# Performance work log

Hardware: AMD Instinct MI355X
Metric: run time of the kernel (lower is better)

Reference implementation:

```python
import jax, jax.numpy as jnp
import numpy as np

B, H, S = 128, 512, 2048

def setup_inputs() -> dict:
    key = jax.random.key(0)
    ks = jax.random.split(key, 8)
    sc = 1.0 / np.sqrt(H)
    return {
        "all_hidden": jax.random.normal(ks[0], (B, H, S), dtype=jnp.float32),
        "v_att": jax.random.normal(ks[1], (H,), dtype=jnp.float32) * sc,
        "W_att": jax.random.normal(ks[2], (H, H), dtype=jnp.float32) * sc,
        "v_ptr": jax.random.normal(ks[3], (H,), dtype=jnp.float32) * sc,
        "fc1_w": jax.random.normal(ks[4], (H, H), dtype=jnp.float32) * sc,
        "fc1_b": jax.random.normal(ks[5], (H,), dtype=jnp.float32) * sc,
        "fc2_w": jax.random.normal(ks[6], (H, H), dtype=jnp.float32) * sc,
        "fc2_b": jax.random.normal(ks[7], (H,), dtype=jnp.float32) * sc,
    }

def reference(all_hidden, v_att, W_att, v_ptr, fc1_w, fc1_b, fc2_w, fc2_b):
    # all_hidden: [B, H, S]
    # Attention: attns = softmax(v . tanh(W @ all_hidden), over seq)
    scores = jnp.einsum('hk,bks->bhs', W_att, all_hidden)          # [B,H,S]
    attn = jax.nn.softmax(jnp.einsum('h,bhs->bs', v_att, jnp.tanh(scores)), axis=-1)  # [B,S]
    # context = attn @ all_hidden^T  -> [B,H]
    context = jnp.einsum('bs,bhs->bh', attn, all_hidden)
    # 2-layer MLP with relu (torch Linear: x @ W^T + b)
    out = jax.nn.relu(context @ fc1_w.T + fc1_b)
    out = jax.nn.relu(out @ fc2_w.T + fc2_b)                        # [B,H]
    # probs = v . tanh(all_hidden + out broadcast over seq)
    probs = jnp.einsum('h,bhs->bs', v_ptr, jnp.tanh(all_hidden + out[:, :, None]))  # [B,S]
    return probs
```

## Files before the change

kernel.cpp:

```cpp
#include <hip/hip_runtime.h>
#include <hip/hip_bf16.h>

#define B_ 128
#define H_ 512
#define S_ 2048
#define ST 64
#define NP (S_/ST)
#define RB 520

typedef short  bf16x8  __attribute__((ext_vector_type(8)));
typedef float  floatx4 __attribute__((ext_vector_type(4)));

__device__ __forceinline__ unsigned short f2bf(float f){
  unsigned u = __float_as_uint(f);
  unsigned r = (u + 0x7fffu + ((u >> 16) & 1u)) >> 16;
  return (unsigned short)r;
}
__device__ __forceinline__ float bf2f(unsigned short h){
  return __uint_as_float(((unsigned)h) << 16);
}
__device__ __forceinline__ float fast_tanh(float x){
  x = fminf(15.f, fmaxf(-15.f, x));
  float e = __expf(2.f * x);
  return (e - 1.f) * __builtin_amdgcn_rcpf(e + 1.f);
}

typedef short short4v __attribute__((ext_vector_type(4)));
__global__ __launch_bounds__(256) void k_convW(const float* __restrict__ W,
                                               unsigned short* __restrict__ Wb){
  int i = (blockIdx.x * 256 + threadIdx.x) * 4;
  float4 v = *(const float4*)(W + i);
  short4v o;
  o[0] = (short)f2bf(v.x); o[1] = (short)f2bf(v.y);
  o[2] = (short)f2bf(v.z); o[3] = (short)f2bf(v.w);
  *(short4v*)(Wb + i) = o;
}

__global__ __launch_bounds__(256, 2) void k_pass1(
    const float* __restrict__ hidden, const float* __restrict__ v_att,
    const unsigned short* __restrict__ Wb,
    float* __restrict__ part_m, float* __restrict__ part_z,
    float* __restrict__ part_ctx)
{
  __shared__ unsigned short Bs[ST * RB];
  __shared__ float vatt[H_];
  __shared__ float twav[4][ST];
  __shared__ float ts[ST];
  __shared__ float es[ST];

  const int tid = threadIdx.x;
  const int w = tid >> 6, l = tid & 63;
  const int p = blockIdx.x & (NP - 1);
  const int b = blockIdx.x >> 5;
  const int s0 = p * ST;

  vatt[tid]       = v_att[tid];
  vatt[tid + 256] = v_att[tid + 256];

  {
    const float* src0 = hidden + ((size_t)b * H_) * S_ + s0 + l;
    #pragma unroll
    for (int it = 0; it < 16; ++it){
      int kb = it * 32 + w * 8;
      const float* src = src0 + (size_t)kb * S_;
      bf16x8 pk;
      #pragma unroll
      for (int j = 0; j < 8; ++j)
        pk[j] = (short)f2bf(src[(size_t)j * S_]);
      *(bf16x8*)(&Bs[l * RB + kb]) = pk;
    }
  }
  __syncthreads();

  const int quad = l >> 4, l16 = l & 15;
  float tacc[4] = {0.f, 0.f, 0.f, 0.f};

  for (int o = 0; o < 2; ++o){
    const int htbase = w * 8 + o * 4;
    floatx4 acc[4][4];
    #pragma unroll
    for (int ti = 0; ti < 4; ++ti)
      #pragma unroll
      for (int ss = 0; ss < 4; ++ss){
        floatx4 z4 = {0.f, 0.f, 0.f, 0.f};
        acc[ti][ss] = z4;
      }

    for (int k0 = 0; k0 < H_; k0 += 32){
      bf16x8 a[4];
      #pragma unroll
      for (int ti = 0; ti < 4; ++ti)
        a[ti] = *(const bf16x8*)(Wb + ((htbase + ti) * 16 + l16) * H_ + k0 + quad * 8);
      bf16x8 bb[4];
      #pragma unroll
      for (int ss = 0; ss < 4; ++ss)
        bb[ss] = *(const bf16x8*)(&Bs[(ss * 16 + l16) * RB + k0 + quad * 8]);
      #pragma unroll
      for (int ti = 0; ti < 4; ++ti)
        #pragma unroll
        for (int ss = 0; ss < 4; ++ss)
          acc[ti][ss] = __builtin_amdgcn_mfma_f32_16x16x32_bf16(a[ti], bb[ss], acc[ti][ss], 0, 0, 0);
    }

    #pragma unroll
    for (int ti = 0; ti < 4; ++ti){
      const int hbase = (htbase + ti) * 16 + quad * 4;
      #pragma unroll
      for (int r = 0; r < 4; ++r){
        float va = vatt[hbase + r];
        #pragma unroll
        for (int ss = 0; ss < 4; ++ss)
          tacc[ss] += va * fast_tanh(acc[ti][ss][r]);
      }
    }
  }

  #pragma unroll
  for (int ss = 0; ss < 4; ++ss){
    tacc[ss] += __shfl_xor(tacc[ss], 16);
    tacc[ss] += __shfl_xor(tacc[ss], 32);
  }
  if (l < 16){
    #pragma unroll
    for (int ss = 0; ss < 4; ++ss) twav[w][ss * 16 + l] = tacc[ss];
  }
  __syncthreads();
  if (tid < ST) ts[tid] = twav[0][tid] + twav[1][tid] + twav[2][tid] + twav[3][tid];
  __syncthreads();

  float m = -1e30f;
  for (int s = 0; s < ST; ++s) m = fmaxf(m, ts[s]);
  if (tid < ST) es[tid] = __expf(ts[tid] - m);
  __syncthreads();
  float z = 0.f;
  for (int s = 0; s < ST; ++s) z += es[s];

  const int pidx = b * NP + p;
  if (tid == 0){ part_m[pidx] = m; part_z[pidx] = z; }

  for (int h = tid; h < H_; h += 256){
    float a = 0.f;
    for (int s = 0; s < ST; ++s) a += es[s] * bf2f(Bs[s * RB + h]);
    part_ctx[(size_t)pidx * H_ + h] = a;
  }
}

__global__ __launch_bounds__(256) void k_mlp(
    const float* __restrict__ part_m, const float* __restrict__ part_z,
    const float* __restrict__ part_ctx,
    const float* __restrict__ fc1_w, const float* __restrict__ fc1_b,
    const float* __restrict__ fc2_w, const float* __restrict__ fc2_b,
    float* __restrict__ out2)
{
  __shared__ float ctx[H_];
  __shared__ float h1[H_];
  __shared__ float wp[NP];
  const int b = blockIdx.x, tid = threadIdx.x;

  float m = -1e30f;
  for (int pp = 0; pp < NP; ++pp) m = fmaxf(m, part_m[b * NP + pp]);
  if (tid < NP) wp[tid] = __expf(part_m[b * NP + tid] - m);
  __syncthreads();
  float z = 0.f;
  for (int pp = 0; pp < NP; ++pp) z += wp[pp] * part_z[b * NP + pp];
  float invz = 1.f / z;

  for (int h = tid; h < H_; h += 256){
    float a = 0.f;
    for (int pp = 0; pp < NP; ++pp) a += wp[pp] * part_ctx[(size_t)(b * NP + pp) * H_ + h];
    ctx[h] = a * invz;
  }
  __syncthreads();

  for (int i = tid; i < H_; i += 256){
    const float4* row = (const float4*)(fc1_w + (size_t)i * H_);
    float4 s4 = {0.f, 0.f, 0.f, 0.f};
    for (int j = 0; j < H_ / 4; ++j){
      float4 wv = row[j];
      s4.x += wv.x * ctx[4 * j];     s4.y += wv.y * ctx[4 * j + 1];
      s4.z += wv.z * ctx[4 * j + 2]; s4.w += wv.w * ctx[4 * j + 3];
    }
    h1[i] = fmaxf(fc1_b[i] + s4.x + s4.y + s4.z + s4.w, 0.f);
  }
  __syncthreads();

  for (int i = tid; i < H_; i += 256){
    const float4* row = (const float4*)(fc2_w + (size_t)i * H_);
    float4 s4 = {0.f, 0.f, 0.f, 0.f};
    for (int j = 0; j < H_ / 4; ++j){
      float4 wv = row[j];
      s4.x += wv.x * h1[4 * j];     s4.y += wv.y * h1[4 * j + 1];
      s4.z += wv.z * h1[4 * j + 2]; s4.w += wv.w * h1[4 * j + 3];
    }
    out2[(size_t)b * H_ + i] = fmaxf(fc2_b[i] + s4.x + s4.y + s4.z + s4.w, 0.f);
  }
}

__global__ __launch_bounds__(256) void k_probs(
    const float* __restrict__ hidden, const float* __restrict__ v_ptr,
    const float* __restrict__ out2, float* __restrict__ probs)
{
  __shared__ float vp[H_], ob[H_];
  const int b = blockIdx.y, c = blockIdx.x, tid = threadIdx.x;
  vp[tid]       = v_ptr[tid];
  vp[tid + 256] = v_ptr[tid + 256];
  ob[tid]       = out2[(size_t)b * H_ + tid];
  ob[tid + 256] = out2[(size_t)b * H_ + tid + 256];
  __syncthreads();

  const int s = c * 512 + tid * 2;
  const float* base = hidden + (size_t)b * H_ * S_ + s;
  float a0 = 0.f, a1 = 0.f;
  #pragma unroll 4
  for (int h = 0; h < H_; ++h){
    float2 hv = *(const float2*)(base + (size_t)h * S_);
    float wv = vp[h], o = ob[h];
    a0 += wv * fast_tanh(hv.x + o);
    a1 += wv * fast_tanh(hv.y + o);
  }
  probs[(size_t)b * S_ + s]     = a0;
  probs[(size_t)b * S_ + s + 1] = a1;
}

extern "C" void kernel_launch(void* const* d_in, const int* in_sizes, int n_in,
                              void* d_out, int out_size, void* d_ws, size_t ws_size,
                              hipStream_t stream)
{
  const float* hidden = (const float*)d_in[0];
  const float* v_att  = (const float*)d_in[1];
  const float* W_att  = (const float*)d_in[2];
  const float* v_ptr  = (const float*)d_in[3];
  const float* fc1_w  = (const float*)d_in[4];
  const float* fc1_b  = (const float*)d_in[5];
  const float* fc2_w  = (const float*)d_in[6];
  const float* fc2_b  = (const float*)d_in[7];
  float* probs = (float*)d_out;

  char* ws = (char*)d_ws;
  unsigned short* Wb = (unsigned short*)ws;
  float* part_m   = (float*)(ws + 524288);
  float* part_z   = (float*)(ws + 524288 + 16384);
  float* part_ctx = (float*)(ws + 524288 + 32768);
  float* out2     = (float*)(ws + 524288 + 32768 + 8388608);

  hipLaunchKernelGGL(k_convW, dim3(256), dim3(256), 0, stream, W_att, Wb);
  hipLaunchKernelGGL(k_pass1, dim3(B_ * NP), dim3(256), 0, stream,
                     hidden, v_att, Wb, part_m, part_z, part_ctx);
  hipLaunchKernelGGL(k_mlp, dim3(B_), dim3(256), 0, stream,
                     part_m, part_z, part_ctx, fc1_w, fc1_b, fc2_w, fc2_b, out2);
  hipLaunchKernelGGL(k_probs, dim3(4, B_), dim3(256), 0, stream,
                     hidden, v_ptr, out2, probs);
}
```

Before: 1.136 ms.

## Pre-transpose hidden to bf16 [B,S,H] and use it in attention and pointer passes

```diff
diff --git a/kernel.cpp b/kernel.cpp
--- a/kernel.cpp
+++ b/kernel.cpp
@@ -10,6 +10,7 @@
 
 typedef short  bf16x8  __attribute__((ext_vector_type(8)));
 typedef float  floatx4 __attribute__((ext_vector_type(4)));
+typedef short  short4v __attribute__((ext_vector_type(4)));
 
 __device__ __forceinline__ unsigned short f2bf(float f){
   unsigned u = __float_as_uint(f);
@@ -25,7 +26,6 @@
   return (e - 1.f) * __builtin_amdgcn_rcpf(e + 1.f);
 }
 
-typedef short short4v __attribute__((ext_vector_type(4)));
 __global__ __launch_bounds__(256) void k_convW(const float* __restrict__ W,
                                                unsigned short* __restrict__ Wb){
   int i = (blockIdx.x * 256 + threadIdx.x) * 4;
@@ -36,26 +36,156 @@
   *(short4v*)(Wb + i) = o;
 }
 
-__global__ __launch_bounds__(256, 2) void k_pass1(
+__global__ __launch_bounds__(256) void k_trans(const float* __restrict__ hidden,
+                                               unsigned short* __restrict__ hT){
+  const int tid = threadIdx.x, w = tid >> 6, l = tid & 63;
+  const int b = blockIdx.y, s0 = blockIdx.x * 64;
+  const float* src = hidden + (size_t)b * H_ * S_ + s0 + l;
+  unsigned short* dst = hT + ((size_t)(b * S_) + s0 + l) * H_;
+  #pragma unroll 4
+  for (int it = 0; it < 16; ++it){
+    int h0 = it * 32 + w * 8;
+    bf16x8 pk;
+    #pragma unroll
+    for (int j = 0; j < 8; ++j)
+      pk[j] = (short)f2bf(src[(size_t)(h0 + j) * S_]);
+    *(bf16x8*)(dst + h0) = pk;
+  }
+}
+
+struct Pass1Shared {
+  unsigned short Bs[ST * RB];
+  float vatt[H_];
+  float twav[4][ST];
+  float ts[ST];
+  float es[ST];
+};
+
+__device__ __forceinline__ void pass1_core(Pass1Shared& sh,
+    const unsigned short* __restrict__ Wb,
+    float* __restrict__ part_m, float* __restrict__ part_z,
+    float* __restrict__ part_ctx, int b, int p)
+{
+  const int tid = threadIdx.x;
+  const int w = tid >> 6, l = tid & 63;
+  const int quad = l >> 4, l16 = l & 15;
+  float tacc[4] = {0.f, 0.f, 0.f, 0.f};
+
+  for (int o = 0; o < 2; ++o){
+    const int htbase = w * 8 + o * 4;
+    floatx4 acc[4][4];
+    #pragma unroll
+    for (int ti = 0; ti < 4; ++ti)
+      #pragma unroll
+      for (int ss = 0; ss < 4; ++ss){
+        floatx4 z4 = {0.f, 0.f, 0.f, 0.f};
+        acc[ti][ss] = z4;
+      }
+
+    for (int k0 = 0; k0 < H_; k0 += 32){
+      bf16x8 a[4];
+      #pragma unroll
+      for (int ti = 0; ti < 4; ++ti)
+        a[ti] = *(const bf16x8*)(Wb + ((htbase + ti) * 16 + l16) * H_ + k0 + quad * 8);
+      bf16x8 bb[4];
+      #pragma unroll
+      for (int ss = 0; ss < 4; ++ss)
+        bb[ss] = *(const bf16x8*)(&sh.Bs[(ss * 16 + l16) * RB + k0 + quad * 8]);
+      #pragma unroll
+      for (int ti = 0; ti < 4; ++ti)
+        #pragma unroll
+        for (int ss = 0; ss < 4; ++ss)
+          acc[ti][ss] = __builtin_amdgcn_mfma_f32_16x16x32_bf16(a[ti], bb[ss], acc[ti][ss], 0, 0, 0);
+    }
+
+    #pragma unroll
+    for (int ti = 0; ti < 4; ++ti){
+      const int hbase = (htbase + ti) * 16 + quad * 4;
+      #pragma unroll
+      for (int r = 0; r < 4; ++r){
+        float va = sh.vatt[hbase + r];
+        #pragma unroll
+        for (int ss = 0; ss < 4; ++ss)
+          tacc[ss] += va * fast_tanh(acc[ti][ss][r]);
+      }
+    }
+  }
+
+  #pragma unroll
+  for (int ss = 0; ss < 4; ++ss){
+    tacc[ss] += __shfl_xor(tacc[ss], 16);
+    tacc[ss] += __shfl_xor(tacc[ss], 32);
+  }
+  if (l < 16){
+    #pragma unroll
+    for (int ss = 0; ss < 4; ++ss) sh.twav[w][ss * 16 + l] = tacc[ss];
+  }
+  __syncthreads();
+  if (tid < ST) sh.ts[tid] = sh.twav[0][tid] + sh.twav[1][tid] + sh.twav[2][tid] + sh.twav[3][tid];
+  __syncthreads();
+
+  float m = -1e30f;
+  for (int s = 0; s < ST; ++s) m = fmaxf(m, sh.ts[s]);
+  if (tid < ST) sh.es[tid] = __expf(sh.ts[tid] - m);
+  __syncthreads();
+  float z = 0.f;
+  for (int s = 0; s < ST; ++s) z += sh.es[s];
+
+  const int pidx = b * NP + p;
+  if (tid == 0){ part_m[pidx] = m; part_z[pidx] = z; }
+
+  for (int h = tid; h < H_; h += 256){
+    float a = 0.f;
+    for (int s = 0; s < ST; ++s) a += sh.es[s] * bf2f(sh.Bs[s * RB + h]);
+    part_ctx[(size_t)pidx * H_ + h] = a;
+  }
+}
+
+__global__ __launch_bounds__(256, 2) void k_pass1_hT(
+    const unsigned short* __restrict__ hT, const float* __restrict__ v_att,
+    const unsigned short* __restrict__ Wb,
+    float* __restrict__ part_m, float* __restrict__ part_z,
+    float* __restrict__ part_ctx)
+{
+  __shared__ Pass1Shared sh;
+  const int tid = threadIdx.x, w = tid >> 6, l = tid & 63;
+  const int p = blockIdx.x & (NP - 1);
+  const int b = blockIdx.x >> 5;
+  const int s0 = p * ST;
+
+  sh.vatt[tid]       = v_att[tid];
+  sh.vatt[tid + 256] = v_att[tid + 256];
+
+  const unsigned short* src = hT + (size_t)(b * S_ + s0) * H_;
+  #pragma unroll
+  for (int r = 0; r < 2; ++r){
+    const int s = w * 16 + (l >> 3) * 2 + r;
+    const unsigned short* row = src + (size_t)s * H_;
+    #pragma unroll
+    for (int i = 0; i < 8; ++i){
+      const int c8 = ((l & 7) + 8 * i) * 8;
+      bf16x8 v = *(const bf16x8*)(row + c8);
+      *(bf16x8*)(&sh.Bs[s * RB + c8]) = v;
+    }
+  }
+  __syncthreads();
+  pass1_core(sh, Wb, part_m, part_z, part_ctx, b, p);
+}
+
+__global__ __launch_bounds__(256, 2) void k_pass1_f32(
     const float* __restrict__ hidden, const float* __restrict__ v_att,
     const unsigned short* __restrict__ Wb,
     float* __restrict__ part_m, float* __restrict__ part_z,
     float* __restrict__ part_ctx)
 {
-  __shared__ unsigned short Bs[ST * RB];
-  __shared__ float vatt[H_];
-  __shared__ float twav[4][ST];
-  __shared__ float ts[ST];
-  __shared__ float es[ST];
-
-  const int tid = threadIdx.x;
-  const int w = tid >> 6, l = tid & 63;
+  __shared__ Pass1Shared sh;
+  const int tid = threadIdx.x, w = tid >> 6, l = tid & 63;
   const int p = blockIdx.x & (NP - 1);
   const int b = blockIdx.x >> 5;
   const int s0 = p * ST;
 
-  vatt[tid]       = v_att[tid];
-  vatt[tid + 256] = v_att[tid + 256];
+  sh.vatt[tid]       = v_att[tid];
+  sh.vatt[tid + 256] = v_att[tid + 256];
 
   {
     const float* src0 = hidden + ((size_t)b * H_) * S_ + s0 + l;
@@ -67,82 +197,11 @@
       #pragma unroll
       for (int j = 0; j < 8; ++j)
         pk[j] = (short)f2bf(src[(size_t)j * S_]);
-      *(bf16x8*)(&Bs[l * RB + kb]) = pk;
-    }
-  }
-  __syncthreads();
-
-  const int quad = l >> 4, l16 = l & 15;
-  float tacc[4] = {0.f, 0.f, 0.f, 0.f};
-
-  for (int o = 0; o < 2; ++o){
-    const int htbase = w * 8 + o * 4;
-    floatx4 acc[4][4];
-    #pragma unroll
-    for (int ti = 0; ti < 4; ++ti)
-      #pragma unroll
-      for (int ss = 0; ss < 4; ++ss){
-        floatx4 z4 = {0.f, 0.f, 0.f, 0.f};
-        acc[ti][ss] = z4;
-      }
-
-    for (int k0 = 0; k0 < H_; k0 += 32){
-      bf16x8 a[4];
-      #pragma unroll
-      for (int ti = 0; ti < 4; ++ti)
-        a[ti] = *(const bf16x8*)(Wb + ((htbase + ti) * 16 + l16) * H_ + k0 + quad * 8);
-      bf16x8 bb[4];
-      #pragma unroll
-      for (int ss = 0; ss < 4; ++ss)
-        bb[ss] = *(const bf16x8*)(&Bs[(ss * 16 + l16) * RB + k0 + quad * 8]);
-      #pragma unroll
-      for (int ti = 0; ti < 4; ++ti)
-        #pragma unroll
-        for (int ss = 0; ss < 4; ++ss)
-          acc[ti][ss] = __builtin_amdgcn_mfma_f32_16x16x32_bf16(a[ti], bb[ss], acc[ti][ss], 0, 0, 0);
-    }
-
-    #pragma unroll
-    for (int ti = 0; ti < 4; ++ti){
-      const int hbase = (htbase + ti) * 16 + quad * 4;
-      #pragma unroll
-      for (int r = 0; r < 4; ++r){
-        float va = vatt[hbase + r];
-        #pragma unroll
-        for (int ss = 0; ss < 4; ++ss)
-          tacc[ss] += va * fast_tanh(acc[ti][ss][r]);
-      }
-    }
-  }
-
-  #pragma unroll
-  for (int ss = 0; ss < 4; ++ss){
-    tacc[ss] += __shfl_xor(tacc[ss], 16);
-    tacc[ss] += __shfl_xor(tacc[ss], 32);
-  }
-  if (l < 16){
-    #pragma unroll
-    for (int ss = 0; ss < 4; ++ss) twav[w][ss * 16 + l] = tacc[ss];
-  }
-  __syncthreads();
-  if (tid < ST) ts[tid] = twav[0][tid] + twav[1][tid] + twav[2][tid] + twav[3][tid];
-  __syncthreads();
-
-  float m = -1e30f;
-  for (int s = 0; s < ST; ++s) m = fmaxf(m, ts[s]);
-  if (tid < ST) es[tid] = __expf(ts[tid] - m);
-  __syncthreads();
-  float z = 0.f;
-  for (int s = 0; s < ST; ++s) z += es[s];
-
-  const int pidx = b * NP + p;
-  if (tid == 0){ part_m[pidx] = m; part_z[pidx] = z; }
-
-  for (int h = tid; h < H_; h += 256){
-    float a = 0.f;
-    for (int s = 0; s < ST; ++s) a += es[s] * bf2f(Bs[s * RB + h]);
-    part_ctx[(size_t)pidx * H_ + h] = a;
-  }
+      *(bf16x8*)(&sh.Bs[l * RB + kb]) = pk;
+    }
+  }
+  __syncthreads();
+  pass1_core(sh, Wb, part_m, part_z, part_ctx, b, p);
 }
 
 __global__ __launch_bounds__(256) void k_mlp(
@@ -196,7 +255,42 @@
   }
 }
 
-__global__ __launch_bounds__(256) void k_probs(
+__global__ __launch_bounds__(256) void k_probs_hT(
+    const unsigned short* __restrict__ hT, const float* __restrict__ v_ptr,
+    const float* __restrict__ out2, float* __restrict__ probs)
+{
+  const int tid = threadIdx.x, w = tid >> 6, l = tid & 63;
+  const int b = blockIdx.y, s0 = blockIdx.x * 64;
+
+  float vp[8], ob[8];
+  {
+    float4 a = *(const float4*)(v_ptr + l * 8);
+    float4 c = *(const float4*)(v_ptr + l * 8 + 4);
+    vp[0]=a.x; vp[1]=a.y; vp[2]=a.z; vp[3]=a.w;
+    vp[4]=c.x; vp[5]=c.y; vp[6]=c.z; vp[7]=c.w;
+    float4 d = *(const float4*)(out2 + (size_t)b * H_ + l * 8);
+    float4 e = *(const float4*)(out2 + (size_t)b * H_ + l * 8 + 4);
+    ob[0]=d.x; ob[1]=d.y; ob[2]=d.z; ob[3]=d.w;
+    ob[4]=e.x; ob[5]=e.y; ob[6]=e.z; ob[7]=e.w;
+  }
+
+  const unsigned short* base = hT + (size_t)(b * S_ + s0) * H_ + l * 8;
+  #pragma unroll 2
+  for (int i = 0; i < 16; ++i){
+    const int s = w * 16 + i;
+    bf16x8 hv = *(const bf16x8*)(base + (size_t)s * H_);
+    float acc = 0.f;
+    #pragma unroll
+    for (int j = 0; j < 8; ++j)
+      acc += vp[j] * fast_tanh(bf2f((unsigned short)hv[j]) + ob[j]);
+    acc += __shfl_xor(acc, 1);  acc += __shfl_xor(acc, 2);
+    acc += __shfl_xor(acc, 4);  acc += __shfl_xor(acc, 8);
+    acc += __shfl_xor(acc, 16); acc += __shfl_xor(acc, 32);
+    if (l == 0) probs[(size_t)b * S_ + s0 + s] = acc;
+  }
+}
+
+__global__ __launch_bounds__(256) void k_probs_f32(
     const float* __restrict__ hidden, const float* __restrict__ v_ptr,
     const float* __restrict__ out2, float* __restrict__ probs)
 {
@@ -238,16 +332,30 @@
 
   char* ws = (char*)d_ws;
   unsigned short* Wb = (unsigned short*)ws;
-  float* part_m   = (float*)(ws + 524288);
-  float* part_z   = (float*)(ws + 524288 + 16384);
-  float* part_ctx = (float*)(ws + 524288 + 32768);
-  float* out2     = (float*)(ws + 524288 + 32768 + 8388608);
+  float* part_m   = (float*)(ws + (512u<<10));
+  float* part_z   = (float*)(ws + (512u<<10) + (16u<<10));
+  float* part_ctx = (float*)(ws + (512u<<10) + (32u<<10));
+  float* out2     = (float*)(ws + (512u<<10) + (32u<<10) + (8u<<20));
+  unsigned short* hT = (unsigned short*)(ws + (16u<<20));
+
+  const size_t need = (16u<<20) + ((size_t)B_ * S_ * H_ * 2);
 
   hipLaunchKernelGGL(k_convW, dim3(256), dim3(256), 0, stream, W_att, Wb);
-  hipLaunchKernelGGL(k_pass1, dim3(B_ * NP), dim3(256), 0, stream,
-                     hidden, v_att, Wb, part_m, part_z, part_ctx);
-  hipLaunchKernelGGL(k_mlp, dim3(B_), dim3(256), 0, stream,
-                     part_m, part_z, part_ctx, fc1_w, fc1_b, fc2_w, fc2_b, out2);
-  hipLaunchKernelGGL(k_probs, dim3(4, B_), dim3(256), 0, stream,
-                     hidden, v_ptr, out2, probs);
-}
+
+  if (ws_size >= need){
+    hipLaunchKernelGGL(k_trans, dim3(S_/64, B_), dim3(256), 0, stream, hidden, hT);
+    hipLaunchKernelGGL(k_pass1_hT, dim3(B_ * NP), dim3(256), 0, stream,
+                       hT, v_att, Wb, part_m, part_z, part_ctx);
+    hipLaunchKernelGGL(k_mlp, dim3(B_), dim3(256), 0, stream,
+                       part_m, part_z, part_ctx, fc1_w, fc1_b, fc2_w, fc2_b, out2);
+    hipLaunchKernelGGL(k_probs_hT, dim3(S_/64, B_), dim3(256), 0, stream,
+                       hT, v_ptr, out2, probs);
+  } else {
+    hipLaunchKernelGGL(k_pass1_f32, dim3(B_ * NP), dim3(256), 0, stream,
+                       hidden, v_att, Wb, part_m, part_z, part_ctx);
+    hipLaunchKernelGGL(k_mlp, dim3(B_), dim3(256), 0, stream,
+                       part_m, part_z, part_ctx, fc1_w, fc1_b, fc2_w, fc2_b, out2);
+    hipLaunchKernelGGL(k_probs_f32, dim3(4, B_), dim3(256), 0, stream,
+                       hidden, v_ptr, out2, probs);
+  }
+}
```

Measured after the change: 1.503 ms. 1.32x slower.

## Write bf16 transposed hidden in pass1 and read it in probs kernel

Applied to the files above, without the earlier changes.

```diff
diff --git a/kernel.cpp b/kernel.cpp
--- a/kernel.cpp
+++ b/kernel.cpp
@@ -6,10 +6,10 @@
 #define S_ 2048
 #define ST 64
 #define NP (S_/ST)
-#define RB 520
 
 typedef short  bf16x8  __attribute__((ext_vector_type(8)));
 typedef float  floatx4 __attribute__((ext_vector_type(4)));
+typedef short  short4v __attribute__((ext_vector_type(4)));
 
 __device__ __forceinline__ unsigned short f2bf(float f){
   unsigned u = __float_as_uint(f);
@@ -24,8 +24,10 @@
   float e = __expf(2.f * x);
   return (e - 1.f) * __builtin_amdgcn_rcpf(e + 1.f);
 }
-
-typedef short short4v __attribute__((ext_vector_type(4)));
+__device__ __forceinline__ int swz(int s, int c){
+  return (c & 56) | ((c ^ s) & 7);
+}
+
 __global__ __launch_bounds__(256) void k_convW(const float* __restrict__ W,
                                                unsigned short* __restrict__ Wb){
   int i = (blockIdx.x * 256 + threadIdx.x) * 4;
@@ -36,15 +38,16 @@
   *(short4v*)(Wb + i) = o;
 }
 
-__global__ __launch_bounds__(256, 2) void k_pass1(
+template<int WRITE_HT>
+__global__ __launch_bounds__(512, 4) void k_pass1(
     const float* __restrict__ hidden, const float* __restrict__ v_att,
     const unsigned short* __restrict__ Wb,
     float* __restrict__ part_m, float* __restrict__ part_z,
-    float* __restrict__ part_ctx)
-{
-  __shared__ unsigned short Bs[ST * RB];
+    float* __restrict__ part_ctx, unsigned short* __restrict__ hT)
+{
+  __shared__ unsigned short Bs[ST * 512];
   __shared__ float vatt[H_];
-  __shared__ float twav[4][ST];
+  __shared__ float twav[8][ST];
   __shared__ float ts[ST];
   __shared__ float es[ST];
 
@@ -54,29 +57,37 @@
   const int b = blockIdx.x >> 5;
   const int s0 = p * ST;
 
-  vatt[tid]       = v_att[tid];
-  vatt[tid + 256] = v_att[tid + 256];
+  vatt[tid] = v_att[tid];
 
   {
     const float* src0 = hidden + ((size_t)b * H_) * S_ + s0 + l;
     #pragma unroll
-    for (int it = 0; it < 16; ++it){
-      int kb = it * 32 + w * 8;
-      const float* src = src0 + (size_t)kb * S_;
+    for (int it = 0; it < 8; ++it){
+      const int c = w + it * 8;
+      const float* src = src0 + (size_t)(c * 8) * S_;
       bf16x8 pk;
       #pragma unroll
       for (int j = 0; j < 8; ++j)
-        pk[j] = (short)f2bf(src[(size_t)j * S_]);
-      *(bf16x8*)(&Bs[l * RB + kb]) = pk;
-    }
-  }
-  __syncthreads();
+        pk[j] = (short)f2bf(__builtin_nontemporal_load(src + (size_t)j * S_));
+      *(bf16x8*)(&Bs[l * 512 + swz(l, c) * 8]) = pk;
+    }
+  }
+  __syncthreads();
+
+  if (WRITE_HT){
+    #pragma unroll
+    for (int r = 0; r < 8; ++r){
+      const int s = w * 8 + r;
+      bf16x8 v = *(const bf16x8*)(&Bs[s * 512 + swz(s, l) * 8]);
+      __builtin_nontemporal_store(v,
+          (bf16x8*)(hT + ((size_t)(b * S_) + s0 + s) * H_ + l * 8));
+    }
+  }
 
   const int quad = l >> 4, l16 = l & 15;
   float tacc[4] = {0.f, 0.f, 0.f, 0.f};
 
-  for (int o = 0; o < 2; ++o){
-    const int htbase = w * 8 + o * 4;
+  {
     floatx4 acc[4][4];
     #pragma unroll
     for (int ti = 0; ti < 4; ++ti)
@@ -90,11 +101,13 @@
       bf16x8 a[4];
       #pragma unroll
       for (int ti = 0; ti < 4; ++ti)
-        a[ti] = *(const bf16x8*)(Wb + ((htbase + ti) * 16 + l16) * H_ + k0 + quad * 8);
+        a[ti] = *(const bf16x8*)(Wb + ((w * 4 + ti) * 16 + l16) * H_ + k0 + quad * 8);
       bf16x8 bb[4];
       #pragma unroll
-      for (int ss = 0; ss < 4; ++ss)
-        bb[ss] = *(const bf16x8*)(&Bs[(ss * 16 + l16) * RB + k0 + quad * 8]);
+      for (int ss = 0; ss < 4; ++ss){
+        const int c = (k0 >> 3) + quad;
+        bb[ss] = *(const bf16x8*)(&Bs[(ss * 16 + l16) * 512 + swz(l16, c) * 8]);
+      }
       #pragma unroll
       for (int ti = 0; ti < 4; ++ti)
         #pragma unroll
@@ -104,7 +117,7 @@
 
     #pragma unroll
     for (int ti = 0; ti < 4; ++ti){
-      const int hbase = (htbase + ti) * 16 + quad * 4;
+      const int hbase = (w * 4 + ti) * 16 + quad * 4;
       #pragma unroll
       for (int r = 0; r < 4; ++r){
         float va = vatt[hbase + r];
@@ -125,7 +138,12 @@
     for (int ss = 0; ss < 4; ++ss) twav[w][ss * 16 + l] = tacc[ss];
   }
   __syncthreads();
-  if (tid < ST) ts[tid] = twav[0][tid] + twav[1][tid] + twav[2][tid] + twav[3][tid];
+  if (tid < ST){
+    float a = 0.f;
+    #pragma unroll
+    for (int ww = 0; ww < 8; ++ww) a += twav[ww][tid];
+    ts[tid] = a;
+  }
   __syncthreads();
 
   float m = -1e30f;
@@ -138,10 +156,12 @@
   const int pidx = b * NP + p;
   if (tid == 0){ part_m[pidx] = m; part_z[pidx] = z; }
 
-  for (int h = tid; h < H_; h += 256){
+  {
+    const int c = tid >> 3, e = tid & 7;
     float a = 0.f;
-    for (int s = 0; s < ST; ++s) a += es[s] * bf2f(Bs[s * RB + h]);
-    part_ctx[(size_t)pidx * H_ + h] = a;
+    for (int s = 0; s < ST; ++s)
+      a += es[s] * bf2f(Bs[s * 512 + swz(s, c) * 8 + e]);
+    part_ctx[(size_t)pidx * H_ + tid] = a;
   }
 }
 
@@ -196,7 +216,42 @@
   }
 }
 
-__global__ __launch_bounds__(256) void k_probs(
+__global__ __launch_bounds__(256) void k_probs_hT(
+    const unsigned short* __restrict__ hT, const float* __restrict__ v_ptr,
+    const float* __restrict__ out2, float* __restrict__ probs)
+{
+  const int tid = threadIdx.x, w = tid >> 6, l = tid & 63;
+  const int b = blockIdx.y, s0 = blockIdx.x * 64;
+
+  float vp[8], ob[8];
+  {
+    float4 a = *(const float4*)(v_ptr + l * 8);
+    float4 c = *(const float4*)(v_ptr + l * 8 + 4);
+    vp[0]=a.x; vp[1]=a.y; vp[2]=a.z; vp[3]=a.w;
+    vp[4]=c.x; vp[5]=c.y; vp[6]=c.z; vp[7]=c.w;
+    float4 d = *(const float4*)(out2 + (size_t)b * H_ + l * 8);
+    float4 e = *(const float4*)(out2 + (size_t)b * H_ + l * 8 + 4);
+    ob[0]=d.x; ob[1]=d.y; ob[2]=d.z; ob[3]=d.w;
+    ob[4]=e.x; ob[5]=e.y; ob[6]=e.z; ob[7]=e.w;
+  }
+
+  const unsigned short* base = hT + (size_t)(b * S_ + s0) * H_ + l * 8;
+  #pragma unroll 2
+  for (int i = 0; i < 16; ++i){
+    const int s = w * 16 + i;
+    bf16x8 hv = __builtin_nontemporal_load((const bf16x8*)(base + (size_t)s * H_));
+    float acc = 0.f;
+    #pragma unroll
+    for (int j = 0; j < 8; ++j)
+      acc += vp[j] * fast_tanh(bf2f((unsigned short)hv[j]) + ob[j]);
+    acc += __shfl_xor(acc, 1);  acc += __shfl_xor(acc, 2);
+    acc += __shfl_xor(acc, 4);  acc += __shfl_xor(acc, 8);
+    acc += __shfl_xor(acc, 16); acc += __shfl_xor(acc, 32);
+    if (l == 0) probs[(size_t)b * S_ + s0 + s] = acc;
+  }
+}
+
+__global__ __launch_bounds__(256) void k_probs_f32(
     const float* __restrict__ hidden, const float* __restrict__ v_ptr,
     const float* __restrict__ out2, float* __restrict__ probs)
 {
@@ -238,16 +293,29 @@
 
   char* ws = (char*)d_ws;
   unsigned short* Wb = (unsigned short*)ws;
-  float* part_m   = (float*)(ws + 524288);
-  float* part_z   = (float*)(ws + 524288 + 16384);
-  float* part_ctx = (float*)(ws + 524288 + 32768);
-  float* out2     = (float*)(ws + 524288 + 32768 + 8388608);
+  float* part_m   = (float*)(ws + (512u<<10));
+  float* part_z   = (float*)(ws + (512u<<10) + (16u<<10));
+  float* part_ctx = (float*)(ws + (512u<<10) + (32u<<10));
+  float* out2     = (float*)(ws + (512u<<10) + (32u<<10) + (8u<<20));
+  unsigned short* hT = (unsigned short*)(ws + (16u<<20));
+
+  const size_t need = (16u<<20) + ((size_t)B_ * S_ * H_ * 2);
 
   hipLaunchKernelGGL(k_convW, dim3(256), dim3(256), 0, stream, W_att, Wb);
-  hipLaunchKernelGGL(k_pass1, dim3(B_ * NP), dim3(256), 0, stream,
-                     hidden, v_att, Wb, part_m, part_z, part_ctx);
-  hipLaunchKernelGGL(k_mlp, dim3(B_), dim3(256), 0, stream,
-                     part_m, part_z, part_ctx, fc1_w, fc1_b, fc2_w, fc2_b, out2);
-  hipLaunchKernelGGL(k_probs, dim3(4, B_), dim3(256), 0, stream,
-                     hidden, v_ptr, out2, probs);
-}
+
+  if (ws_size >= need){
+    hipLaunchKernelGGL(k_pass1<1>, dim3(B_ * NP), dim3(512), 0, stream,
+                       hidden, v_att, Wb, part_m, part_z, part_ctx, hT);
+    hipLaunchKernelGGL(k_mlp, dim3(B_), dim3(256), 0, stream,
+                       part_m, part_z, part_ctx, fc1_w, fc1_b, fc2_w, fc2_b, out2);
+    hipLaunchKernelGGL(k_probs_hT, dim3(S_/64, B_), dim3(256), 0, stream,
+                       hT, v_ptr, out2, probs);
+  } else {
+    hipLaunchKernelGGL(k_pass1<0>, dim3(B_ * NP), dim3(512), 0, stream,
+                       hidden, v_att, Wb, part_m, part_z, part_ctx, (unsigned short*)Wb);
+    hipLaunchKernelGGL(k_mlp, dim3(B_), dim3(256), 0, stream,
+                       part_m, part_z, part_ctx, fc1_w, fc1_b, fc2_w, fc2_b, out2);
+    hipLaunchKernelGGL(k_probs_f32, dim3(4, B_), dim3(256), 0, stream,
+                       hidden, v_ptr, out2, probs);
+  }
+}
```

Result: faster. 1.039 ms (-8.5%).
